# Kernel tuning notes

Measured on AMD Instinct MI355X. Metric: run time of the kernel, lower is better.

## Reference

```python
import jax, jax.numpy as jnp
import numpy as np

LN_EPS = 1e-5


def _mlp(x, W1, b1, W2, b2, g, beta):
    # build_mlp_d: Linear -> ReLU -> Linear -> LayerNorm (mlp_layers=2, lay_norm=True)
    h = jax.nn.relu(x @ W1 + b1)
    h = h @ W2 + b2
    mu = jnp.mean(h, axis=-1, keepdims=True)
    var = jnp.var(h, axis=-1, keepdims=True)
    return (h - mu) * jax.lax.rsqrt(var + LN_EPS) * g + beta


def setup_inputs() -> dict:
    E, N, L, EIF = 524288, 65536, 128, 3
    key = jax.random.key(0)
    ks = iter(jax.random.split(key, 48))
    def rn(shape, s=1.0):
        return jax.random.normal(next(ks), shape, dtype=jnp.float32) * s
    inp = {}
    inp["edge_index"] = jax.random.randint(next(ks), (2, E), 0, N)
    inp["edge_dx_"] = rn((E, 3))
    inp["edge_attr"] = rn((E, EIF))
    for nm in ["vector_a", "vector_b", "vector_c",
               "senders_v_t_", "senders_v_tm1_", "senders_w_t_", "senders_w_tm1_",
               "senders_a_t_", "senders_alpha_t_",
               "receivers_v_t_", "receivers_v_tm1_", "receivers_w_t_", "receivers_w_tm1_",
               "receivers_a_t_", "receivers_alpha_t_"]:
        inp[nm] = rn((E, 3))
    inp["node_latent"] = rn((N, L))
    def mlp_params(pfx, din):
        inp[pfx + "_W1"] = rn((din, L), 0.05)
        inp[pfx + "_b1"] = jnp.zeros((L,), jnp.float32)
        inp[pfx + "_W2"] = rn((L, L), 0.05)
        inp[pfx + "_b2"] = jnp.zeros((L,), jnp.float32)
        inp[pfx + "_g"] = jnp.ones((L,), jnp.float32)
        inp[pfx + "_beta"] = jnp.zeros((L,), jnp.float32)
    mlp_params("fe", 18)        # edge_feat_encoder
    mlp_params("ee", 1 + EIF)   # edge_encoder
    mlp_params("ie", 3 * L)     # interaction_encoder
    return inp


def reference(edge_index, edge_dx_, edge_attr, vector_a, vector_b, vector_c,
              senders_v_t_, senders_v_tm1_, senders_w_t_, senders_w_tm1_,
              senders_a_t_, senders_alpha_t_,
              receivers_v_t_, receivers_v_tm1_, receivers_w_t_, receivers_w_tm1_,
              receivers_a_t_, receivers_alpha_t_,
              node_latent,
              fe_W1, fe_b1, fe_W2, fe_b2, fe_g, fe_beta,
              ee_W1, ee_b1, ee_W2, ee_b2, ee_g, ee_beta,
              ie_W1, ie_b1, ie_W2, ie_b2, ie_g, ie_beta):
    senders, receivers = edge_index[0], edge_index[1]
    basis = jnp.stack([vector_a, vector_b, vector_c], axis=1)  # [E,3,3]
    # Fuse the 12 small bmm projections into two batched einsums.
    s_stack = jnp.stack([senders_v_t_, senders_v_tm1_, senders_w_t_, senders_w_tm1_,
                         senders_a_t_, senders_alpha_t_], axis=1)   # [E,6,3]
    r_stack = jnp.stack([receivers_v_t_, receivers_v_tm1_, receivers_w_t_, receivers_w_tm1_,
                         receivers_a_t_, receivers_alpha_t_], axis=1)
    s_proj = jnp.einsum('eij,ekj->eki', basis, s_stack)  # [E,6,3]
    r_proj = jnp.einsum('eij,ekj->eki', basis, r_stack)
    # signs: -v_t, -v_tm1, -w_t, +w_tm1, -a_t, +alpha_t (receivers side)
    r_sign = jnp.array([-1.0, -1.0, -1.0, 1.0, -1.0, 1.0], jnp.float32)[None, :, None]
    E = s_proj.shape[0]
    senders_features = s_proj.reshape(E, 18)
    receivers_features = (r_proj * r_sign).reshape(E, 18)
    edge_dx_norm = jnp.linalg.norm(edge_dx_, axis=1, keepdims=True)  # [E,1]
    edge_latent = _mlp(jnp.concatenate([edge_dx_norm, edge_attr], axis=1),
                       ee_W1, ee_b1, ee_W2, ee_b2, ee_g, ee_beta)
    senders_latent = _mlp(senders_features, fe_W1, fe_b1, fe_W2, fe_b2, fe_g, fe_beta)
    receivers_latent = _mlp(receivers_features, fe_W1, fe_b1, fe_W2, fe_b2, fe_g, fe_beta)
    node_sum = node_latent[senders] + node_latent[receivers]  # [E,L]
    msg_input = jnp.concatenate([senders_latent + receivers_latent, node_sum, edge_latent], axis=1)
    return _mlp(msg_input, ie_W1, ie_b1, ie_W2, ie_b2, ie_g, ie_beta)
```

## Files before the change

### kernel.cpp

```cpp
#include <hip/hip_runtime.h>

typedef __attribute__((ext_vector_type(4))) float fx4;
typedef __attribute__((ext_vector_type(8))) unsigned short u16x8;
typedef __attribute__((ext_vector_type(8))) __bf16 bf16x8;

static __device__ __forceinline__ unsigned short f2bf(float f) {
  unsigned int u = __builtin_bit_cast(unsigned int, f);
  u += 0x7fffu + ((u >> 16) & 1u);
  return (unsigned short)(u >> 16);
}
static __device__ __forceinline__ fx4 mfma16(u16x8 a, u16x8 b, fx4 c) {
  return __builtin_amdgcn_mfma_f32_16x16x32_bf16(
      __builtin_bit_cast(bf16x8, a), __builtin_bit_cast(bf16x8, b), c, 0, 0, 0);
}

static __device__ __forceinline__ int swz128(int row, int col) {
  return row * 128 + (col ^ ((row & 7) << 3));
}
static __device__ __forceinline__ int swz32(int row, int col) {
  return row * 32 + (col ^ (((row >> 1) & 3) << 3));
}

#define WT_FE1 0
#define WT_FE2 4096
#define WT_EE1 20480
#define WT_EE2 24576
#define WT_A   40960
#define WT_B   57344
#define WT_C   73728
#define WT_IE2 90112
#define WT_TOTAL 106496

__global__ void prep_weights(const float* __restrict__ feW1, const float* __restrict__ feW2,
                             const float* __restrict__ eeW1, const float* __restrict__ eeW2,
                             const float* __restrict__ ieW1, const float* __restrict__ ieW2,
                             unsigned short* __restrict__ wt) {
  int i = blockIdx.x * 256 + threadIdx.x;
  if (i >= WT_TOTAL) return;
  int base, n, k, kpad;
  float val;
  if (i < WT_FE2)      { base = WT_FE1; n = i >> 5; k = i & 31; kpad = 32;
                         val = (k < 18) ? feW1[k * 128 + n] : 0.f; }
  else if (i < WT_EE1) { base = WT_FE2; int j = i - WT_FE2; n = j >> 7; k = j & 127; kpad = 128;
                         val = feW2[k * 128 + n]; }
  else if (i < WT_EE2) { base = WT_EE1; int j = i - WT_EE1; n = j >> 5; k = j & 31; kpad = 32;
                         val = (k < 4) ? eeW1[k * 128 + n] : 0.f; }
  else if (i < WT_A)   { base = WT_EE2; int j = i - WT_EE2; n = j >> 7; k = j & 127; kpad = 128;
                         val = eeW2[k * 128 + n]; }
  else if (i < WT_B)   { base = WT_A;   int j = i - WT_A;   n = j >> 7; k = j & 127; kpad = 128;
                         val = ieW1[k * 128 + n]; }
  else if (i < WT_C)   { base = WT_B;   int j = i - WT_B;   n = j >> 7; k = j & 127; kpad = 128;
                         val = ieW1[(128 + k) * 128 + n]; }
  else if (i < WT_IE2) { base = WT_C;   int j = i - WT_C;   n = j >> 7; k = j & 127; kpad = 128;
                         val = ieW1[(256 + k) * 128 + n]; }
  else                 { base = WT_IE2; int j = i - WT_IE2; n = j >> 7; k = j & 127; kpad = 128;
                         val = ieW2[k * 128 + n]; }
  int dst = (kpad == 32) ? base + n * 32 + (k ^ (((n >> 1) & 3) << 3))
                         : base + n * 128 + (k ^ ((n & 7) << 3));
  wt[dst] = f2bf(val);
}

template<int KPAD, int KT>
static __device__ __forceinline__ void gemm_lds(const unsigned short* As,
                                                const unsigned short* Ws,
                                                fx4* acc, int l16, int lgr) {
#pragma unroll
  for (int kk = 0; kk < KT; kk++) {
    const int k0 = kk * 32 + lgr * 8;
    u16x8 af = *(const u16x8*)(As + ((KPAD == 32) ? swz32(l16, k0) : swz128(l16, k0)));
#pragma unroll
    for (int nt = 0; nt < 8; nt++) {
      const int n = nt * 16 + l16;
      u16x8 bf = *(const u16x8*)(Ws + ((KPAD == 32) ? swz32(n, k0) : swz128(n, k0)));
      acc[nt] = mfma16(af, bf, acc[nt]);
    }
  }
}

static __device__ __forceinline__ void relu_store(fx4* acc, const float* __restrict__ bias,
                                                  unsigned short* dst, int l16, int lgr) {
#pragma unroll
  for (int nt = 0; nt < 8; nt++) {
    const int col = nt * 16 + l16;
    const float b = bias[col];
#pragma unroll
    for (int r = 0; r < 4; r++) {
      float v = acc[nt][r] + b;
      dst[swz128(lgr * 4 + r, col)] = f2bf(v > 0.f ? v : 0.f);
    }
  }
}

static __device__ __forceinline__ void ln_rows(fx4* acc, const float* __restrict__ bias, int l16) {
  float sum[4] = {0, 0, 0, 0}, sq[4] = {0, 0, 0, 0};
#pragma unroll
  for (int nt = 0; nt < 8; nt++) {
    const float b = bias[nt * 16 + l16];
#pragma unroll
    for (int r = 0; r < 4; r++) {
      float v = acc[nt][r] + b; acc[nt][r] = v;
      sum[r] += v; sq[r] += v * v;
    }
  }
#pragma unroll
  for (int r = 0; r < 4; r++) {
    float s_ = sum[r], q_ = sq[r];
#pragma unroll
    for (int m = 1; m < 16; m <<= 1) { s_ += __shfl_xor(s_, m, 64); q_ += __shfl_xor(q_, m, 64); }
    const float mu = s_ * (1.f / 128.f);
    const float rs = rsqrtf(q_ * (1.f / 128.f) - mu * mu + 1e-5f);
#pragma unroll
    for (int nt = 0; nt < 8; nt++) acc[nt][r] = (acc[nt][r] - mu) * rs;
  }
}

struct ParamsFE {
  const float* basis[3];
  const float* sv[6]; const float* rv[6];
  const float* b1; const float* b2; const float* g; const float* be;
};
struct ParamsEE {
  const float* dx; const float* attr;
  const float* b1; const float* b2; const float* g; const float* be;
};

static __device__ __forceinline__ void fe_body(const ParamsFE& p, unsigned short* lds,
                                               const unsigned short* wt, unsigned short* msg,
                                               int bid, int nblocks, int ntiles) {
  const int tid = threadIdx.x;
  const int wave = tid >> 6, lane = tid & 63;
  const int l16 = lane & 15, lgr = lane >> 4;
#pragma unroll
  for (int i = tid * 8; i < 20480; i += 4096)
    *(u16x8*)(lds + i) = *(const u16x8*)(wt + WT_FE1 + i);
  const unsigned short* W1 = lds;
  const unsigned short* W2 = lds + 4096;
  unsigned short* h1 = lds + 20480 + wave * 2560;
  unsigned short* feat = h1 + 2048;
  __syncthreads();
#pragma unroll
  for (int j = 0; j < 4; j++) { int c = 18 + lgr * 4 + j; if (c < 32) feat[swz32(l16, c)] = 0; }
  const fx4 z4 = {0.f, 0.f, 0.f, 0.f};

  for (int t = bid; t < ntiles; t += nblocks) {
    const int e0 = t * 128 + wave * 16;
    const size_t e = (size_t)(e0 + l16);
    float bx[3][3];
#pragma unroll
    for (int i = 0; i < 3; i++) {
      const float* bp = p.basis[i] + 3 * e;
      bx[i][0] = bp[0]; bx[i][1] = bp[1]; bx[i][2] = bp[2];
    }
    fx4 latS[8];
#pragma unroll
    for (int side = 0; side < 2; side++) {
      const bool isR = (side == 1);
#pragma unroll
      for (int k = 0; k < 6; k++) {
        if ((k & 3) == lgr) {
          const float* vp = (isR ? p.rv[k] : p.sv[k]) + 3 * e;
          const float v0 = vp[0], v1 = vp[1], v2 = vp[2];
          const float sgn = (isR && k != 3 && k != 5) ? -1.f : 1.f;
#pragma unroll
          for (int i = 0; i < 3; i++) {
            float d = (bx[i][0] * v0 + bx[i][1] * v1 + bx[i][2] * v2) * sgn;
            feat[swz32(l16, k * 3 + i)] = f2bf(d);
          }
        }
      }
      fx4 acc[8];
#pragma unroll
      for (int b = 0; b < 8; b++) acc[b] = z4;
      gemm_lds<32, 1>(feat, W1, acc, l16, lgr);
      relu_store(acc, p.b1, h1, l16, lgr);
#pragma unroll
      for (int b = 0; b < 8; b++) acc[b] = z4;
      gemm_lds<128, 4>(h1, W2, acc, l16, lgr);
      ln_rows(acc, p.b2, l16);
      if (!isR) {
#pragma unroll
        for (int nt = 0; nt < 8; nt++) {
          const int col = nt * 16 + l16;
          const float gg = p.g[col], bb = p.be[col];
#pragma unroll
          for (int r = 0; r < 4; r++) latS[nt][r] = acc[nt][r] * gg + bb;
        }
      } else {
#pragma unroll
        for (int nt = 0; nt < 8; nt++) {
          const int col = nt * 16 + l16;
          const float gg = p.g[col], bb = p.be[col];
#pragma unroll
          for (int r = 0; r < 4; r++)
            msg[(size_t)(e0 + lgr * 4 + r) * 256 + col] =
                f2bf(latS[nt][r] + acc[nt][r] * gg + bb);
        }
      }
    }
  }
}

static __device__ __forceinline__ void ee_body(const ParamsEE& p, unsigned short* lds,
                                               const unsigned short* wt, unsigned short* msg,
                                               int bid, int nblocks, int ntiles) {
  const int tid = threadIdx.x;
  const int wave = tid >> 6, lane = tid & 63;
  const int l16 = lane & 15, lgr = lane >> 4;
#pragma unroll
  for (int i = tid * 8; i < 20480; i += 4096)
    *(u16x8*)(lds + i) = *(const u16x8*)(wt + WT_EE1 + i);
  const unsigned short* W1 = lds;
  const unsigned short* W2 = lds + 4096;
  unsigned short* h1 = lds + 20480 + wave * 2560;
  unsigned short* feat = h1 + 2048;
  __syncthreads();
#pragma unroll
  for (int j = 0; j < 7; j++) feat[swz32(l16, 4 + lgr * 7 + j)] = 0;
  const fx4 z4 = {0.f, 0.f, 0.f, 0.f};

  for (int t = bid; t < ntiles; t += nblocks) {
    const int e0 = t * 128 + wave * 16;
    const size_t e = (size_t)(e0 + l16);
    if (lgr == 0) {
      float d0 = p.dx[3 * e], d1 = p.dx[3 * e + 1], d2 = p.dx[3 * e + 2];
      feat[swz32(l16, 0)] = f2bf(sqrtf(d0 * d0 + d1 * d1 + d2 * d2));
    } else {
      feat[swz32(l16, lgr)] = f2bf(p.attr[3 * e + (lgr - 1)]);
    }
    fx4 acc[8];
#pragma unroll
    for (int b = 0; b < 8; b++) acc[b] = z4;
    gemm_lds<32, 1>(feat, W1, acc, l16, lgr);
    relu_store(acc, p.b1, h1, l16, lgr);
#pragma unroll
    for (int b = 0; b < 8; b++) acc[b] = z4;
    gemm_lds<128, 4>(h1, W2, acc, l16, lgr);
    ln_rows(acc, p.b2, l16);
#pragma unroll
    for (int nt = 0; nt < 8; nt++) {
      const int col = nt * 16 + l16;
      const float gg = p.g[col], bb = p.be[col];
#pragma unroll
      for (int r = 0; r < 4; r++)
        msg[(size_t)(e0 + lgr * 4 + r) * 256 + 128 + col] =
            f2bf(acc[nt][r] * gg + bb);
    }
  }
}

__global__ __launch_bounds__(512) void feee_kernel(ParamsFE pf, ParamsEE pe,
                                                   const unsigned short* wt,
                                                   unsigned short* msg,
                                                   int nfe, int ntiles) {
  extern __shared__ unsigned short lds[];
  if ((int)blockIdx.x < nfe)
    fe_body(pf, lds, wt, msg, blockIdx.x, nfe, ntiles);
  else
    ee_body(pe, lds, wt, msg, blockIdx.x - nfe, gridDim.x - nfe, ntiles);
}

struct ParamsIE {
  const int* eidx;
  const float* nl;
  const float* b1; const float* b2; const float* g; const float* be;
  const unsigned short* wt;
  const unsigned short* msg;
  float* out;
  int E; int nt16;
};

__global__ __launch_bounds__(768, 3) void ie_kernel(ParamsIE p) {
  extern __shared__ unsigned short dyn[];
  const int tid = threadIdx.x;
  const int wave = tid >> 6, lane = tid & 63;
  const int l16 = lane & 15, lgr = lane >> 4;
  for (int i = tid * 8; i < 49152; i += 6144)
    *(u16x8*)(dyn + i) = *(const u16x8*)(p.wt + WT_A + i);
  const unsigned short* WA = dyn;
  const unsigned short* WB = dyn + 16384;
  const unsigned short* WC = dyn + 32768;
  unsigned short* h1 = dyn + 49152 + wave * 2048;
  __syncthreads();
  const fx4 z4 = {0.f, 0.f, 0.f, 0.f};

  const int gw = blockIdx.x * 12 + wave;
  const int gstride = gridDim.x * 12;
  for (int t = gw; t < p.nt16; t += gstride) {
    const int e0 = t * 16;
    const size_t e = (size_t)(e0 + l16);
    const int sidx = p.eidx[e];
    const int ridx = p.eidx[(size_t)p.E + e];
    const unsigned short* mrow = p.msg + e * 256;
    const float* ns = p.nl + (size_t)sidx * 128;
    const float* nr = p.nl + (size_t)ridx * 128;
    fx4 acc[8];
#pragma unroll
    for (int b = 0; b < 8; b++) acc[b] = z4;
#pragma unroll
    for (int c = 0; c < 4; c++) {
      const int k0 = c * 32 + lgr * 8;
      fx4 a0 = *(const fx4*)(ns + k0), a1 = *(const fx4*)(ns + k0 + 4);
      fx4 b0 = *(const fx4*)(nr + k0), b1 = *(const fx4*)(nr + k0 + 4);
      u16x8 af;
#pragma unroll
      for (int j = 0; j < 4; j++) { af[j] = f2bf(a0[j] + b0[j]); af[4 + j] = f2bf(a1[j] + b1[j]); }
#pragma unroll
      for (int nt = 0; nt < 8; nt++) {
        u16x8 bf = *(const u16x8*)(WB + swz128(nt * 16 + l16, k0));
        acc[nt] = mfma16(af, bf, acc[nt]);
      }
    }
#pragma unroll
    for (int c = 0; c < 4; c++) {
      const int k0 = c * 32 + lgr * 8;
      u16x8 af = *(const u16x8*)(mrow + k0);
#pragma unroll
      for (int nt = 0; nt < 8; nt++) {
        u16x8 bf = *(const u16x8*)(WA + swz128(nt * 16 + l16, k0));
        acc[nt] = mfma16(af, bf, acc[nt]);
      }
    }
#pragma unroll
    for (int c = 0; c < 4; c++) {
      const int k0 = c * 32 + lgr * 8;
      u16x8 af = *(const u16x8*)(mrow + 128 + k0);
#pragma unroll
      for (int nt = 0; nt < 8; nt++) {
        u16x8 bf = *(const u16x8*)(WC + swz128(nt * 16 + l16, k0));
        acc[nt] = mfma16(af, bf, acc[nt]);
      }
    }
    relu_store(acc, p.b1, h1, l16, lgr);
#pragma unroll
    for (int b = 0; b < 8; b++) acc[b] = z4;
    gemm_lds<128, 4>(h1, p.wt + WT_IE2, acc, l16, lgr);
    ln_rows(acc, p.b2, l16);
#pragma unroll
    for (int nt = 0; nt < 8; nt++) {
      const int col = nt * 16 + l16;
      const float gg = p.g[col], bb = p.be[col];
#pragma unroll
      for (int r = 0; r < 4; r++)
        p.out[(size_t)(e0 + lgr * 4 + r) * 128 + col] = acc[nt][r] * gg + bb;
    }
  }
}

extern "C" void kernel_launch(void* const* d_in, const int* in_sizes, int n_in,
                              void* d_out, int out_size, void* d_ws, size_t ws_size,
                              hipStream_t stream) {
  (void)n_in; (void)out_size;
  const int E = in_sizes[1] / 3;
  unsigned short* wt = reinterpret_cast<unsigned short*>(d_ws);
  if (ws_size < (size_t)WT_TOTAL * sizeof(unsigned short)) return;

  prep_weights<<<(WT_TOTAL + 255) / 256, 256, 0, stream>>>(
      (const float*)d_in[19], (const float*)d_in[21],
      (const float*)d_in[25], (const float*)d_in[27],
      (const float*)d_in[31], (const float*)d_in[33], wt);

  unsigned short* msg = (unsigned short*)d_out;

  hipFuncSetAttribute((const void*)feee_kernel,
                      hipFuncAttributeMaxDynamicSharedMemorySize, 81920);
  hipFuncSetAttribute((const void*)ie_kernel,
                      hipFuncAttributeMaxDynamicSharedMemorySize, 147456);

  ParamsFE pf;
  for (int i = 0; i < 3; i++) pf.basis[i] = (const float*)d_in[3 + i];
  for (int k = 0; k < 6; k++) { pf.sv[k] = (const float*)d_in[6 + k]; pf.rv[k] = (const float*)d_in[12 + k]; }
  pf.b1 = (const float*)d_in[20]; pf.b2 = (const float*)d_in[22];
  pf.g  = (const float*)d_in[23]; pf.be = (const float*)d_in[24];

  ParamsEE pe;
  pe.dx = (const float*)d_in[1]; pe.attr = (const float*)d_in[2];
  pe.b1 = (const float*)d_in[26]; pe.b2 = (const float*)d_in[28];
  pe.g  = (const float*)d_in[29]; pe.be = (const float*)d_in[30];

  feee_kernel<<<1024, 512, 81920, stream>>>(pf, pe, wt, msg, 512, E / 128);

  ParamsIE pi;
  pi.eidx = (const int*)d_in[0];
  pi.nl = (const float*)d_in[18];
  pi.b1 = (const float*)d_in[32]; pi.b2 = (const float*)d_in[34];
  pi.g  = (const float*)d_in[35]; pi.be = (const float*)d_in[36];
  pi.wt = wt; pi.msg = msg; pi.out = (float*)d_out;
  pi.E = E; pi.nt16 = E / 16;
  ie_kernel<<<256, 768, 147456, stream>>>(pi);
}
```

Before: 639.0 us.

## Process 32 edges per wave in ie_kernel to reuse weight fragments across two tiles

Each wave now handles two 16-edge tiles at once, so every weight fragment read feeds two MFMAs instead of one. The WB and IE2 weights are read straight from global memory (through cache) rather than LDS, which frees LDS for a larger per-wave h1 buffer. Launch changes to 512 threads with one block per CU and 128KB of LDS. This doubles accumulator register pressure and lowers wave occupancy, and the global-memory weight reads may add latency.

```diff
diff --git a/kernel.cpp b/kernel.cpp
--- a/kernel.cpp
+++ b/kernel.cpp
@@ -266,82 +266,113 @@
   const unsigned short* wt;
   const unsigned short* msg;
   float* out;
-  int E; int nt16;
+  int E; int nt32;
 };
 
-__global__ __launch_bounds__(768, 3) void ie_kernel(ParamsIE p) {
+__global__ __launch_bounds__(512, 1) void ie_kernel(ParamsIE p) {
   extern __shared__ unsigned short dyn[];
   const int tid = threadIdx.x;
   const int wave = tid >> 6, lane = tid & 63;
   const int l16 = lane & 15, lgr = lane >> 4;
-  for (int i = tid * 8; i < 49152; i += 6144)
+#pragma unroll
+  for (int i = tid * 8; i < 16384; i += 4096) {
     *(u16x8*)(dyn + i) = *(const u16x8*)(p.wt + WT_A + i);
+    *(u16x8*)(dyn + 16384 + i) = *(const u16x8*)(p.wt + WT_C + i);
+  }
   const unsigned short* WA = dyn;
-  const unsigned short* WB = dyn + 16384;
-  const unsigned short* WC = dyn + 32768;
-  unsigned short* h1 = dyn + 49152 + wave * 2048;
+  const unsigned short* WC = dyn + 16384;
+  unsigned short* h1 = dyn + 32768 + wave * 4096;
   __syncthreads();
   const fx4 z4 = {0.f, 0.f, 0.f, 0.f};
 
-  const int gw = blockIdx.x * 12 + wave;
-  const int gstride = gridDim.x * 12;
-  for (int t = gw; t < p.nt16; t += gstride) {
-    const int e0 = t * 16;
-    const size_t e = (size_t)(e0 + l16);
-    const int sidx = p.eidx[e];
-    const int ridx = p.eidx[(size_t)p.E + e];
-    const unsigned short* mrow = p.msg + e * 256;
-    const float* ns = p.nl + (size_t)sidx * 128;
-    const float* nr = p.nl + (size_t)ridx * 128;
-    fx4 acc[8];
-#pragma unroll
-    for (int b = 0; b < 8; b++) acc[b] = z4;
+  const int gw = blockIdx.x * 8 + wave;
+  const int gstride = gridDim.x * 8;
+  for (int t = gw; t < p.nt32; t += gstride) {
+    const int e0 = t * 32;
+    const size_t eA = (size_t)(e0 + l16);
+    const size_t eB = (size_t)(e0 + 16 + l16);
+    const int sA = p.eidx[eA], rA = p.eidx[(size_t)p.E + eA];
+    const int sB = p.eidx[eB], rB = p.eidx[(size_t)p.E + eB];
+    const unsigned short* mrowA = p.msg + eA * 256;
+    const unsigned short* mrowB = p.msg + eB * 256;
+    const float* nsA = p.nl + (size_t)sA * 128;
+    const float* nrA = p.nl + (size_t)rA * 128;
+    const float* nsB = p.nl + (size_t)sB * 128;
+    const float* nrB = p.nl + (size_t)rB * 128;
+    fx4 accA[8], accB[8];
+#pragma unroll
+    for (int b = 0; b < 8; b++) { accA[b] = z4; accB[b] = z4; }
 #pragma unroll
     for (int c = 0; c < 4; c++) {
       const int k0 = c * 32 + lgr * 8;
-      fx4 a0 = *(const fx4*)(ns + k0), a1 = *(const fx4*)(ns + k0 + 4);
-      fx4 b0 = *(const fx4*)(nr + k0), b1 = *(const fx4*)(nr + k0 + 4);
-      u16x8 af;
-#pragma unroll
-      for (int j = 0; j < 4; j++) { af[j] = f2bf(a0[j] + b0[j]); af[4 + j] = f2bf(a1[j] + b1[j]); }
+      fx4 a0 = *(const fx4*)(nsA + k0), a1 = *(const fx4*)(nsA + k0 + 4);
+      fx4 b0 = *(const fx4*)(nrA + k0), b1 = *(const fx4*)(nrA + k0 + 4);
+      fx4 c0 = *(const fx4*)(nsB + k0), c1 = *(const fx4*)(nsB + k0 + 4);
+      fx4 d0 = *(const fx4*)(nrB + k0), d1 = *(const fx4*)(nrB + k0 + 4);
+      u16x8 afA, afB;
+#pragma unroll
+      for (int j = 0; j < 4; j++) {
+        afA[j] = f2bf(a0[j] + b0[j]); afA[4 + j] = f2bf(a1[j] + b1[j]);
+        afB[j] = f2bf(c0[j] + d0[j]); afB[4 + j] = f2bf(c1[j] + d1[j]);
+      }
 #pragma unroll
       for (int nt = 0; nt < 8; nt++) {
-        u16x8 bf = *(const u16x8*)(WB + swz128(nt * 16 + l16, k0));
-        acc[nt] = mfma16(af, bf, acc[nt]);
+        u16x8 bf = *(const u16x8*)(p.wt + WT_B + swz128(nt * 16 + l16, k0));
+        accA[nt] = mfma16(afA, bf, accA[nt]);
+        accB[nt] = mfma16(afB, bf, accB[nt]);
       }
     }
 #pragma unroll
     for (int c = 0; c < 4; c++) {
       const int k0 = c * 32 + lgr * 8;
-      u16x8 af = *(const u16x8*)(mrow + k0);
+      u16x8 afA = *(const u16x8*)(mrowA + k0);
+      u16x8 afB = *(const u16x8*)(mrowB + k0);
 #pragma unroll
       for (int nt = 0; nt < 8; nt++) {
         u16x8 bf = *(const u16x8*)(WA + swz128(nt * 16 + l16, k0));
-        acc[nt] = mfma16(af, bf, acc[nt]);
+        accA[nt] = mfma16(afA, bf, accA[nt]);
+        accB[nt] = mfma16(afB, bf, accB[nt]);
       }
     }
 #pragma unroll
     for (int c = 0; c < 4; c++) {
       const int k0 = c * 32 + lgr * 8;
-      u16x8 af = *(const u16x8*)(mrow + 128 + k0);
+      u16x8 afA = *(const u16x8*)(mrowA + 128 + k0);
+      u16x8 afB = *(const u16x8*)(mrowB + 128 + k0);
 #pragma unroll
       for (int nt = 0; nt < 8; nt++) {
         u16x8 bf = *(const u16x8*)(WC + swz128(nt * 16 + l16, k0));
-        acc[nt] = mfma16(af, bf, acc[nt]);
-      }
-    }
-    relu_store(acc, p.b1, h1, l16, lgr);
-#pragma unroll
-    for (int b = 0; b < 8; b++) acc[b] = z4;
-    gemm_lds<128, 4>(h1, p.wt + WT_IE2, acc, l16, lgr);
-    ln_rows(acc, p.b2, l16);
+        accA[nt] = mfma16(afA, bf, accA[nt]);
+        accB[nt] = mfma16(afB, bf, accB[nt]);
+      }
+    }
+    relu_store(accA, p.b1, h1, l16, lgr);
+    relu_store(accB, p.b1, h1 + 2048, l16, lgr);
+#pragma unroll
+    for (int b = 0; b < 8; b++) { accA[b] = z4; accB[b] = z4; }
+#pragma unroll
+    for (int c = 0; c < 4; c++) {
+      const int k0 = c * 32 + lgr * 8;
+      u16x8 afA = *(const u16x8*)(h1 + swz128(l16, k0));
+      u16x8 afB = *(const u16x8*)(h1 + 2048 + swz128(l16, k0));
+#pragma unroll
+      for (int nt = 0; nt < 8; nt++) {
+        u16x8 bf = *(const u16x8*)(p.wt + WT_IE2 + swz128(nt * 16 + l16, k0));
+        accA[nt] = mfma16(afA, bf, accA[nt]);
+        accB[nt] = mfma16(afB, bf, accB[nt]);
+      }
+    }
+    ln_rows(accA, p.b2, l16);
+    ln_rows(accB, p.b2, l16);
 #pragma unroll
     for (int nt = 0; nt < 8; nt++) {
       const int col = nt * 16 + l16;
       const float gg = p.g[col], bb = p.be[col];
 #pragma unroll
-      for (int r = 0; r < 4; r++)
-        p.out[(size_t)(e0 + lgr * 4 + r) * 128 + col] = acc[nt][r] * gg + bb;
+      for (int r = 0; r < 4; r++) {
+        p.out[(size_t)(e0 + lgr * 4 + r) * 128 + col] = accA[nt][r] * gg + bb;
+        p.out[(size_t)(e0 + 16 + lgr * 4 + r) * 128 + col] = accB[nt][r] * gg + bb;
+      }
     }
   }
 }
@@ -364,7 +395,7 @@
   hipFuncSetAttribute((const void*)feee_kernel,
                       hipFuncAttributeMaxDynamicSharedMemorySize, 81920);
   hipFuncSetAttribute((const void*)ie_kernel,
-                      hipFuncAttributeMaxDynamicSharedMemorySize, 147456);
+                      hipFuncAttributeMaxDynamicSharedMemorySize, 131072);
 
   ParamsFE pf;
   for (int i = 0; i < 3; i++) pf.basis[i] = (const float*)d_in[3 + i];
@@ -385,6 +416,6 @@
   pi.b1 = (const float*)d_in[32]; pi.b2 = (const float*)d_in[34];
   pi.g  = (const float*)d_in[35]; pi.be = (const float*)d_in[36];
   pi.wt = wt; pi.msg = msg; pi.out = (float*)d_out;
-  pi.E = E; pi.nt16 = E / 16;
-  ie_kernel<<<256, 768, 147456, stream>>>(pi);
-}
+  pi.E = E; pi.nt32 = E / 32;
+  ie_kernel<<<256, 512, 131072, stream>>>(pi);
+}
```

Measured after the change: 624.2 us. -2.3%, faster.
